# Kernel optimization log

Measured on AMD Instinct MI355X. Metric: run time of the kernel, lower is better.

The kernel has to match this reference:

```python
import jax, jax.numpy as jnp
import numpy as np

N = 100000      # n_nodes
E = 1600000     # n_edges (avg degree 16)
F_IN = 128      # nfeat
H = 128         # nhid
C = 64          # nclass


def setup_inputs() -> dict:
    key = jax.random.key(0)
    ks = jax.random.split(key, 6)
    x = jax.random.normal(ks[0], (N, F_IN), dtype=jnp.float32)
    edge_index = jax.random.randint(ks[1], (2, E), 0, N, dtype=jnp.int32)
    # Glorot-ish init for GCNConv weights, zeros for bias (PyG default)
    W1 = jax.random.normal(ks[2], (F_IN, H), dtype=jnp.float32) * (1.0 / np.sqrt(F_IN))
    b1 = jnp.zeros((H,), dtype=jnp.float32)
    W2 = jax.random.normal(ks[3], (H, C), dtype=jnp.float32) * (1.0 / np.sqrt(H))
    b2 = jnp.zeros((C,), dtype=jnp.float32)
    return {"x": x, "edge_index": edge_index, "W1": W1, "b1": b1, "W2": W2, "b2": b2}


def _gcn_conv(x, W, b, src, dst, n):
    """PyG GCNConv: h = W^T x, out_i = sum_j norm_ij * h_j + b, with
    symmetric normalization over the self-loop-augmented graph."""
    h = x @ W                                                   # [n, out]
    deg = jax.ops.segment_sum(jnp.ones(src.shape[0], h.dtype), dst, num_segments=n)
    dinv = jnp.where(deg > 0, jax.lax.rsqrt(deg), 0.0)          # D^-1/2
    norm = dinv[src] * dinv[dst]                                # [E+n]
    msg = h[src] * norm[:, None]                                # gather + scale
    out = jax.ops.segment_sum(msg, dst, num_segments=n)         # scatter-add
    return out + b


def reference(x, edge_index, W1, b1, W2, b2):
    loop = jnp.arange(N, dtype=edge_index.dtype)
    src = jnp.concatenate([edge_index[0], loop])  # sources j (with self loops)
    dst = jnp.concatenate([edge_index[1], loop])  # targets i
    h = jax.nn.relu(_gcn_conv(x, W1, b1, src, dst, N))  # dropout = identity (eval)
    out = _gcn_conv(h, W2, b2, src, dst, N)
    return jax.nn.log_softmax(out, axis=1)
```

## Files before the change

kernel.cpp:

```cpp
#include <hip/hip_runtime.h>
#include <hip/hip_fp16.h>
#include <cstdint>
#include <cstddef>
#include <cstring>


__device__ inline unsigned pack_bf16x2(float a, float b) {
    unsigned ua = __float_as_uint(a);
    unsigned ub = __float_as_uint(b);
    ua += 0x7fffu + ((ua >> 16) & 1u);
    ub += 0x7fffu + ((ub >> 16) & 1u);
    return (ua >> 16) | (ub & 0xffff0000u);
}
__device__ inline unsigned short bf16_rne(float v) {
    unsigned u = __float_as_uint(v);
    u += 0x7fffu + ((u >> 16) & 1u);
    return (unsigned short)(u >> 16);
}
__device__ inline float bf16lo(unsigned u) { return __uint_as_float(u << 16); }
__device__ inline float bf16hi(unsigned u) { return __uint_as_float(u & 0xffff0000u); }


typedef float fv2 __attribute__((ext_vector_type(2)));

template <bool HI>
__device__ inline fv2 fp8_fv2(unsigned u) {
#if __has_builtin(__builtin_amdgcn_cvt_pk_f32_fp8)
    return __builtin_amdgcn_cvt_pk_f32_fp8((int)u, HI);
#else
    unsigned u2 = HI ? (u >> 16) : (u & 0xffffu);
    unsigned w = (u2 & 0xFFu) | ((u2 & 0xFF00u) << 8);
    unsigned hb = ((w & 0x00800080u) << 8) | ((w & 0x007f007fu) << 7);
    __half2 h2;
    memcpy(&h2, &hb, 4);
    float2 f = __half22float2(h2);
    fv2 r;
    r.x = f.x * 256.0f;
    r.y = f.y * 256.0f;
    return r;
#endif
}

__device__ inline fv2 bfpair(unsigned u) {
    union { unsigned q[2]; fv2 f; } t;
    t.q[0] = u << 16;
    t.q[1] = u & 0xffff0000u;
    return t.f;
}

__device__ inline unsigned f32_to_fp8_byte(float v) {
    unsigned short hb = __half_as_ushort(__float2half(v * 0.00390625f));
    unsigned t = hb & 0x7fffu;
    t += 0x3fu + ((t >> 7) & 1u);
    return ((hb >> 8) & 0x80u) | (t >> 7);
}

__device__ inline unsigned char f32_to_fp8_b(float v) {
#if __has_builtin(__builtin_amdgcn_cvt_pk_fp8_f32)
    return (unsigned char)(__builtin_amdgcn_cvt_pk_fp8_f32(v, v, 0, false) & 0xff);
#else
    return (unsigned char)f32_to_fp8_byte(v);
#endif
}

typedef int iv4 __attribute__((ext_vector_type(4)));

#define NPART 8
#define KB    32
#define NPP_MAX 12500


__global__ void k_zero16(int* __restrict__ p) {
    if (threadIdx.x < 16) p[threadIdx.x] = 0;
}

__global__ __launch_bounds__(256) void k_bcount(const int* __restrict__ dst,
                                                int* __restrict__ bucketCount,
                                                int E, int npp) {
    __shared__ int c8[NPART];
    if (threadIdx.x < NPART) c8[threadIdx.x] = 0;
    __syncthreads();
    int t = blockIdx.x * blockDim.x + threadIdx.x;
    int stride = gridDim.x * blockDim.x;
    int E4 = E >> 2;
    const iv4* d4 = (const iv4*)dst;
    for (int i = t; i < E4; i += stride) {
        iv4 d = d4[i];
        atomicAdd(&c8[(unsigned)d.x / (unsigned)npp], 1);
        atomicAdd(&c8[(unsigned)d.y / (unsigned)npp], 1);
        atomicAdd(&c8[(unsigned)d.z / (unsigned)npp], 1);
        atomicAdd(&c8[(unsigned)d.w / (unsigned)npp], 1);
    }
    for (int e = E4 * 4 + t; e < E; e += stride)
        atomicAdd(&c8[(unsigned)dst[e] / (unsigned)npp], 1);
    __syncthreads();
    if (threadIdx.x < NPART) atomicAdd(&bucketCount[threadIdx.x], c8[threadIdx.x]);
}

__global__ void k_bscan(const int* __restrict__ bucketCount,
                        int* __restrict__ bucketBase,
                        int* __restrict__ bucketCursor) {
    if (threadIdx.x == 0) {
        int run = 0;
        for (int p = 0; p < NPART; ++p) {
            bucketBase[p] = run;
            bucketCursor[p] = run;
            run += bucketCount[p];
        }
    }
}

__global__ __launch_bounds__(256) void k_bucket(const int* __restrict__ src,
                                                const int* __restrict__ dst,
                                                int* __restrict__ bucketCursor,
                                                int2* __restrict__ pairs,
                                                int E, int npp) {
    __shared__ int cnt8[NPART], run8[NPART], gbase8[NPART];
    int tid = threadIdx.x;
    int base_e = blockIdx.x * 4096 + tid * 16;
    int nv = min(16, E - base_e);
    if (nv < 0) nv = 0;
    int dv[16], sv[16];
    if (nv == 16) {
        for (int q = 0; q < 4; ++q) {
            iv4 d = *(const iv4*)(dst + base_e + q * 4);
            iv4 s = *(const iv4*)(src + base_e + q * 4);
            dv[q * 4 + 0] = d.x; dv[q * 4 + 1] = d.y; dv[q * 4 + 2] = d.z; dv[q * 4 + 3] = d.w;
            sv[q * 4 + 0] = s.x; sv[q * 4 + 1] = s.y; sv[q * 4 + 2] = s.z; sv[q * 4 + 3] = s.w;
        }
    } else {
        for (int k = 0; k < nv; ++k) { dv[k] = dst[base_e + k]; sv[k] = src[base_e + k]; }
    }
    if (tid < NPART) { cnt8[tid] = 0; run8[tid] = 0; }
    __syncthreads();
    for (int k = 0; k < nv; ++k)
        atomicAdd(&cnt8[(unsigned)dv[k] / (unsigned)npp], 1);
    __syncthreads();
    if (tid < NPART) gbase8[tid] = atomicAdd(&bucketCursor[tid], cnt8[tid]);
    __syncthreads();
    for (int k = 0; k < nv; ++k) {
        int p = (unsigned)dv[k] / (unsigned)npp;
        int r = atomicAdd(&run8[p], 1);
        int2 pr; pr.x = dv[k]; pr.y = sv[k];
        pairs[gbase8[p] + r] = pr;
    }
}

__global__ __launch_bounds__(256) void k_count_part(const int2* __restrict__ pairs,
                                                    const int* __restrict__ bucketBase,
                                                    const int* __restrict__ bucketCount,
                                                    int* __restrict__ cntarr, int npp) {
    __shared__ int h[NPP_MAX];
    int p = blockIdx.x & (NPART - 1);
    int b = blockIdx.x >> 3;
    int lo = p * npp;
    for (int i = threadIdx.x; i < npp; i += 256) h[i] = 0;
    __syncthreads();
    int segBase = bucketBase[p], sz = bucketCount[p];
    int chunk = (sz + KB - 1) / KB;
    int s0 = segBase + b * chunk;
    int s1 = min(segBase + sz, s0 + chunk);
    for (int i = s0 + threadIdx.x; i < s1; i += 256)
        atomicAdd(&h[pairs[i].x - lo], 1);
    __syncthreads();
    size_t out = (size_t)(p * KB + b) * npp;
    for (int i = threadIdx.x; i < npp; i += 256) cntarr[out + i] = h[i];
}

__global__ void k_indeg(const int* __restrict__ cntarr, int* __restrict__ indeg,
                        int n, int npp) {
    int d = blockIdx.x * blockDim.x + threadIdx.x;
    if (d >= n) return;
    int p = (unsigned)d / (unsigned)npp;
    int dl = d - p * npp;
    size_t base = (size_t)p * KB * npp + dl;
    int s = 0;
    for (int b = 0; b < KB; ++b) s += cntarr[base + (size_t)b * npp];
    indeg[d] = s;
}

__global__ void k_scan_local(const int* __restrict__ in, int* __restrict__ out,
                             int* __restrict__ partials, int n) {
    __shared__ int s[256];
    int t = threadIdx.x;
    int base = blockIdx.x * 1024 + t * 4;
    int v0 = (base + 0) < n ? in[base + 0] : 0;
    int v1 = (base + 1) < n ? in[base + 1] : 0;
    int v2 = (base + 2) < n ? in[base + 2] : 0;
    int v3 = (base + 3) < n ? in[base + 3] : 0;
    int sum = v0 + v1 + v2 + v3;
    s[t] = sum;
    __syncthreads();
    for (int off = 1; off < 256; off <<= 1) {
        int x = (t >= off) ? s[t - off] : 0;
        __syncthreads();
        s[t] += x;
        __syncthreads();
    }
    int excl = s[t] - sum;
    if ((base + 0) < n) out[base + 0] = excl;
    if ((base + 1) < n) out[base + 1] = excl + v0;
    if ((base + 2) < n) out[base + 2] = excl + v0 + v1;
    if ((base + 3) < n) out[base + 3] = excl + v0 + v1 + v2;
    if (t == 255) partials[blockIdx.x] = s[255];
}

__global__ void k_scan_partials(int* __restrict__ partials, int np) {
    __shared__ int s[256];
    int t = threadIdx.x;
    int v = (t < np) ? partials[t] : 0;
    s[t] = v;
    __syncthreads();
    for (int off = 1; off < 256; off <<= 1) {
        int x = (t >= off) ? s[t - off] : 0;
        __syncthreads();
        s[t] += x;
        __syncthreads();
    }
    if (t < np) partials[t] = s[t] - v;
}

__global__ void k_finalize(int* __restrict__ row_ptr, const int* __restrict__ partials,
                           const int* __restrict__ indeg, float* __restrict__ dinv,
                           int n, int E) {
    int i = blockIdx.x * blockDim.x + threadIdx.x;
    if (i < n) {
        int rp = row_ptr[i] + partials[i >> 10];
        row_ptr[i] = rp;
        dinv[i] = rsqrtf((float)indeg[i] + 1.0f);
        if (i == 0) row_ptr[n] = E;
    }
}

__global__ void k_bases(int* __restrict__ cntarr, const int* __restrict__ row_ptr,
                        int n, int npp) {
    int d = blockIdx.x * blockDim.x + threadIdx.x;
    if (d >= n) return;
    int p = (unsigned)d / (unsigned)npp;
    int dl = d - p * npp;
    size_t base = (size_t)p * KB * npp + dl;
    int run = row_ptr[d];
    for (int b = 0; b < KB; ++b) {
        size_t idx = base + (size_t)b * npp;
        int c = cntarr[idx];
        cntarr[idx] = run;
        run += c;
    }
}

__global__ __launch_bounds__(256) void k_fill2(const int2* __restrict__ pairs,
                                               const int* __restrict__ bucketBase,
                                               const int* __restrict__ bucketCount,
                                               const int* __restrict__ cntarr,
                                               int* __restrict__ col, int npp) {
    __shared__ int cur[NPP_MAX];
    int p = blockIdx.x & (NPART - 1);
    int b = blockIdx.x >> 3;
    int lo = p * npp;
    size_t slice = (size_t)(p * KB + b) * npp;
    for (int i = threadIdx.x; i < npp; i += 256) cur[i] = cntarr[slice + i];
    __syncthreads();
    int segBase = bucketBase[p], sz = bucketCount[p];
    int chunk = (sz + KB - 1) / KB;
    int s0 = segBase + b * chunk;
    int s1 = min(segBase + sz, s0 + chunk);
    for (int i = s0 + threadIdx.x; i < s1; i += 256) {
        int2 e = pairs[i];
        int pos = atomicAdd(&cur[e.x - lo], 1);
        col[pos] = e.y;
    }
}

typedef __attribute__((ext_vector_type(8))) short short8;
typedef __attribute__((ext_vector_type(4))) float f32x4;

union FragU {
    short8 s;
    uint4 u4;
    unsigned u[4];
};

template <int NOUT>
__global__ void k_packW(const float* __restrict__ W, unsigned* __restrict__ Bp) {
    const int NT = NOUT / 16;
    int nf = 4 * NT * 64;
    for (int fid = threadIdx.x; fid < nf; fid += 256) {
        int q = fid / (NT * 64);
        int rem = fid - q * NT * 64;
        int nt = rem >> 6;
        int lane = rem & 63;
        int k0 = q * 32 + (lane >> 4) * 8;
        int ncol = nt * 16 + (lane & 15);
        unsigned u[4];
        for (int h = 0; h < 4; ++h) {
            float a = W[(k0 + 2 * h) * NOUT + ncol];
            float b = W[(k0 + 2 * h + 1) * NOUT + ncol];
            u[h] = pack_bf16x2(a, b);
        }
        uint4 o = {u[0], u[1], u[2], u[3]};
        *(uint4*)(Bp + (size_t)fid * 4) = o;
    }
}

__global__ __launch_bounds__(256) void k_gemm128_mfma(const float* __restrict__ X,
                                                      const unsigned* __restrict__ Bp,
                                                      const float* __restrict__ dinv,
                                                      unsigned char* __restrict__ H8,
                                                      int n) {
    int w = threadIdx.x >> 6;
    int lane = threadIdx.x & 63;
    int quad = lane >> 4;
    int lrow = lane & 15;
    int row0 = blockIdx.x * 64 + w * 16;
    int rowA = min(row0 + lrow, n - 1);

    f32x4 acc[8];
    for (int nt = 0; nt < 8; ++nt) acc[nt] = (f32x4){0.f, 0.f, 0.f, 0.f};

    for (int q = 0; q < 4; ++q) {
        const float* xp = X + (size_t)rowA * 128 + q * 32 + quad * 8;
        float4 x0 = *(const float4*)xp;
        float4 x1 = *(const float4*)(xp + 4);
        FragU a;
        a.u[0] = pack_bf16x2(x0.x, x0.y);
        a.u[1] = pack_bf16x2(x0.z, x0.w);
        a.u[2] = pack_bf16x2(x1.x, x1.y);
        a.u[3] = pack_bf16x2(x1.z, x1.w);
        for (int nt = 0; nt < 8; ++nt) {
            FragU b;
            b.u4 = *(const uint4*)(Bp + ((size_t)(q * 8 + nt) * 64 + lane) * 4);
            acc[nt] = __builtin_amdgcn_mfma_f32_16x16x32_bf16(a.s, b.s, acc[nt], 0, 0, 0);
        }
    }

    int rbase = row0 + quad * 4;
    float dv[4];
    if (rbase + 3 < n) {
        float4 d4 = *(const float4*)(dinv + rbase);
        dv[0] = d4.x; dv[1] = d4.y; dv[2] = d4.z; dv[3] = d4.w;
    } else {
        for (int r = 0; r < 4; ++r) dv[r] = dinv[min(rbase + r, n - 1)];
    }
    for (int nt = 0; nt < 8; ++nt) {
        for (int r = 0; r < 4; ++r) {
            int row = rbase + r;
            if (row < n)
                H8[(size_t)row * 128 + nt * 16 + lrow] = f32_to_fp8_b(dv[r] * acc[nt][r]);
        }
    }
}

__global__ __launch_bounds__(256) void k_gemm64_mfma(const unsigned* __restrict__ Xb,
                                                     const unsigned* __restrict__ Bp,
                                                     const float* __restrict__ dinv,
                                                     unsigned short* __restrict__ H16,
                                                     int n) {
    int w = threadIdx.x >> 6;
    int lane = threadIdx.x & 63;
    int quad = lane >> 4;
    int lrow = lane & 15;
    int row0 = blockIdx.x * 64 + w * 16;
    int rowA = min(row0 + lrow, n - 1);

    f32x4 acc[4];
    for (int nt = 0; nt < 4; ++nt) acc[nt] = (f32x4){0.f, 0.f, 0.f, 0.f};

    for (int q = 0; q < 4; ++q) {
        FragU a;
        a.u4 = *(const uint4*)(Xb + (size_t)rowA * 64 + q * 16 + quad * 4);
        for (int nt = 0; nt < 4; ++nt) {
            FragU b;
            b.u4 = *(const uint4*)(Bp + ((size_t)(q * 4 + nt) * 64 + lane) * 4);
            acc[nt] = __builtin_amdgcn_mfma_f32_16x16x32_bf16(a.s, b.s, acc[nt], 0, 0, 0);
        }
    }

    int rbase = row0 + quad * 4;
    float dv[4];
    if (rbase + 3 < n) {
        float4 d4 = *(const float4*)(dinv + rbase);
        dv[0] = d4.x; dv[1] = d4.y; dv[2] = d4.z; dv[3] = d4.w;
    } else {
        for (int r = 0; r < 4; ++r) dv[r] = dinv[min(rbase + r, n - 1)];
    }
    for (int nt = 0; nt < 4; ++nt) {
        for (int r = 0; r < 4; ++r) {
            int row = rbase + r;
            if (row < n)
                H16[(size_t)row * 64 + nt * 16 + lrow] = bf16_rne(dv[r] * acc[nt][r]);
        }
    }
}


__global__ __launch_bounds__(256) void k_agg_relu(const unsigned* __restrict__ hs,
                                                  const float* __restrict__ dinv,
                                                  const int* __restrict__ row_ptr,
                                                  const int* __restrict__ col,
                                                  const float* __restrict__ bias,
                                                  unsigned* __restrict__ out, int n) {
    int node = blockIdx.x * 16 + (threadIdx.x >> 4);
    if (node >= n) return;
    int l = threadIdx.x & 15;
    const uint2* hrow = (const uint2*)hs;
    fv2 a0 = {0.f, 0.f}, a1 = {0.f, 0.f}, a2 = {0.f, 0.f}, a3 = {0.f, 0.f};
    {
        uint2 u = hrow[(size_t)node * 16 + l];
        a0 += fp8_fv2<false>(u.x); a1 += fp8_fv2<true>(u.x);
        a2 += fp8_fv2<false>(u.y); a3 += fp8_fv2<true>(u.y);
    }
    int k = row_ptr[node], p1 = row_ptr[node + 1];
    for (; k + 8 <= p1; k += 8) {
        int cA = col[k + 0], cB = col[k + 1], cC = col[k + 2], cD = col[k + 3];
        int cE = col[k + 4], cF = col[k + 5], cG = col[k + 6], cH = col[k + 7];
        uint2 uA = hrow[(size_t)cA * 16 + l];
        uint2 uB = hrow[(size_t)cB * 16 + l];
        uint2 uC = hrow[(size_t)cC * 16 + l];
        uint2 uD = hrow[(size_t)cD * 16 + l];
        uint2 uE = hrow[(size_t)cE * 16 + l];
        uint2 uF = hrow[(size_t)cF * 16 + l];
        uint2 uG = hrow[(size_t)cG * 16 + l];
        uint2 uH = hrow[(size_t)cH * 16 + l];
        a0 += fp8_fv2<false>(uA.x); a1 += fp8_fv2<true>(uA.x);
        a2 += fp8_fv2<false>(uA.y); a3 += fp8_fv2<true>(uA.y);
        a0 += fp8_fv2<false>(uB.x); a1 += fp8_fv2<true>(uB.x);
        a2 += fp8_fv2<false>(uB.y); a3 += fp8_fv2<true>(uB.y);
        a0 += fp8_fv2<false>(uC.x); a1 += fp8_fv2<true>(uC.x);
        a2 += fp8_fv2<false>(uC.y); a3 += fp8_fv2<true>(uC.y);
        a0 += fp8_fv2<false>(uD.x); a1 += fp8_fv2<true>(uD.x);
        a2 += fp8_fv2<false>(uD.y); a3 += fp8_fv2<true>(uD.y);
        a0 += fp8_fv2<false>(uE.x); a1 += fp8_fv2<true>(uE.x);
        a2 += fp8_fv2<false>(uE.y); a3 += fp8_fv2<true>(uE.y);
        a0 += fp8_fv2<false>(uF.x); a1 += fp8_fv2<true>(uF.x);
        a2 += fp8_fv2<false>(uF.y); a3 += fp8_fv2<true>(uF.y);
        a0 += fp8_fv2<false>(uG.x); a1 += fp8_fv2<true>(uG.x);
        a2 += fp8_fv2<false>(uG.y); a3 += fp8_fv2<true>(uG.y);
        a0 += fp8_fv2<false>(uH.x); a1 += fp8_fv2<true>(uH.x);
        a2 += fp8_fv2<false>(uH.y); a3 += fp8_fv2<true>(uH.y);
    }
    for (; k + 4 <= p1; k += 4) {
        int cA = col[k + 0], cB = col[k + 1], cC = col[k + 2], cD = col[k + 3];
        uint2 uA = hrow[(size_t)cA * 16 + l];
        uint2 uB = hrow[(size_t)cB * 16 + l];
        uint2 uC = hrow[(size_t)cC * 16 + l];
        uint2 uD = hrow[(size_t)cD * 16 + l];
        a0 += fp8_fv2<false>(uA.x); a1 += fp8_fv2<true>(uA.x);
        a2 += fp8_fv2<false>(uA.y); a3 += fp8_fv2<true>(uA.y);
        a0 += fp8_fv2<false>(uB.x); a1 += fp8_fv2<true>(uB.x);
        a2 += fp8_fv2<false>(uB.y); a3 += fp8_fv2<true>(uB.y);
        a0 += fp8_fv2<false>(uC.x); a1 += fp8_fv2<true>(uC.x);
        a2 += fp8_fv2<false>(uC.y); a3 += fp8_fv2<true>(uC.y);
        a0 += fp8_fv2<false>(uD.x); a1 += fp8_fv2<true>(uD.x);
        a2 += fp8_fv2<false>(uD.y); a3 += fp8_fv2<true>(uD.y);
    }
    for (; k < p1; ++k) {
        int j = col[k];
        uint2 u = hrow[(size_t)j * 16 + l];
        a0 += fp8_fv2<false>(u.x); a1 += fp8_fv2<true>(u.x);
        a2 += fp8_fv2<false>(u.y); a3 += fp8_fv2<true>(u.y);
    }
    float di = dinv[node];
    float4 b4a = *(const float4*)(bias + 8 * l);
    float4 b4b = *(const float4*)(bias + 8 * l + 4);
    float v0 = fmaf(di, a0.x, b4a.x);
    float v1 = fmaf(di, a0.y, b4a.y);
    float v2 = fmaf(di, a1.x, b4a.z);
    float v3 = fmaf(di, a1.y, b4a.w);
    float v4 = fmaf(di, a2.x, b4b.x);
    float v5 = fmaf(di, a2.y, b4b.y);
    float v6 = fmaf(di, a3.x, b4b.z);
    float v7 = fmaf(di, a3.y, b4b.w);
    v0 = v0 > 0.f ? v0 : 0.f;
    v1 = v1 > 0.f ? v1 : 0.f;
    v2 = v2 > 0.f ? v2 : 0.f;
    v3 = v3 > 0.f ? v3 : 0.f;
    v4 = v4 > 0.f ? v4 : 0.f;
    v5 = v5 > 0.f ? v5 : 0.f;
    v6 = v6 > 0.f ? v6 : 0.f;
    v7 = v7 > 0.f ? v7 : 0.f;
    uint4 o = {pack_bf16x2(v0, v1), pack_bf16x2(v2, v3),
               pack_bf16x2(v4, v5), pack_bf16x2(v6, v7)};
    *(uint4*)(out + (size_t)node * 64 + 4 * l) = o;
}

__global__ __launch_bounds__(256) void k_agg_lsm(const unsigned* __restrict__ hs,
                                                 const float* __restrict__ dinv,
                                                 const int* __restrict__ row_ptr,
                                                 const int* __restrict__ col,
                                                 const float* __restrict__ bias,
                                                 float* __restrict__ out, int n) {
    int node = blockIdx.x * 16 + (threadIdx.x >> 4);
    if (node >= n) return;
    int l = threadIdx.x & 15;
    const uint2* hrow = (const uint2*)hs;
    fv2 aX = {0.f, 0.f}, aY = {0.f, 0.f};
    {
        uint2 u = hrow[(size_t)node * 16 + l];
        aX += bfpair(u.x);
        aY += bfpair(u.y);
    }
    int k = row_ptr[node], p1 = row_ptr[node + 1];
    for (; k + 8 <= p1; k += 8) {
        int cA = col[k + 0], cB = col[k + 1], cC = col[k + 2], cD = col[k + 3];
        int cE = col[k + 4], cF = col[k + 5], cG = col[k + 6], cH = col[k + 7];
        uint2 uA = hrow[(size_t)cA * 16 + l];
        uint2 uB = hrow[(size_t)cB * 16 + l];
        uint2 uC = hrow[(size_t)cC * 16 + l];
        uint2 uD = hrow[(size_t)cD * 16 + l];
        uint2 uE = hrow[(size_t)cE * 16 + l];
        uint2 uF = hrow[(size_t)cF * 16 + l];
        uint2 uG = hrow[(size_t)cG * 16 + l];
        uint2 uH = hrow[(size_t)cH * 16 + l];
        aX += bfpair(uA.x); aY += bfpair(uA.y);
        aX += bfpair(uB.x); aY += bfpair(uB.y);
        aX += bfpair(uC.x); aY += bfpair(uC.y);
        aX += bfpair(uD.x); aY += bfpair(uD.y);
        aX += bfpair(uE.x); aY += bfpair(uE.y);
        aX += bfpair(uF.x); aY += bfpair(uF.y);
        aX += bfpair(uG.x); aY += bfpair(uG.y);
        aX += bfpair(uH.x); aY += bfpair(uH.y);
    }
    for (; k + 4 <= p1; k += 4) {
        int cA = col[k + 0], cB = col[k + 1], cC = col[k + 2], cD = col[k + 3];
        uint2 uA = hrow[(size_t)cA * 16 + l];
        uint2 uB = hrow[(size_t)cB * 16 + l];
        uint2 uC = hrow[(size_t)cC * 16 + l];
        uint2 uD = hrow[(size_t)cD * 16 + l];
        aX += bfpair(uA.x); aY += bfpair(uA.y);
        aX += bfpair(uB.x); aY += bfpair(uB.y);
        aX += bfpair(uC.x); aY += bfpair(uC.y);
        aX += bfpair(uD.x); aY += bfpair(uD.y);
    }
    for (; k < p1; ++k) {
        int j = col[k];
        uint2 u = hrow[(size_t)j * 16 + l];
        aX += bfpair(u.x); aY += bfpair(u.y);
    }
    float di = dinv[node];
    float4 b4 = *(const float4*)(bias + 4 * l);
    float v0 = fmaf(di, aX.x, b4.x);
    float v1 = fmaf(di, aX.y, b4.y);
    float v2 = fmaf(di, aY.x, b4.z);
    float v3 = fmaf(di, aY.y, b4.w);
    float m = fmaxf(fmaxf(v0, v1), fmaxf(v2, v3));
    for (int off = 8; off; off >>= 1) m = fmaxf(m, __shfl_xor(m, off));
    float s = __expf(v0 - m) + __expf(v1 - m) + __expf(v2 - m) + __expf(v3 - m);
    for (int off = 8; off; off >>= 1) s += __shfl_xor(s, off);
    float ls = __logf(s);
    float4 o = {v0 - m - ls, v1 - m - ls, v2 - m - ls, v3 - m - ls};
    *(float4*)(out + (size_t)node * 64 + 4 * l) = o;
}


extern "C" void kernel_launch(void* const* d_in, const int* in_sizes, int n_in,
                              void* d_out, int out_size, void* d_ws, size_t ws_size,
                              hipStream_t stream) {
    const float* x  = (const float*)d_in[0];
    const int*   ei = (const int*)d_in[1];
    const float* W1 = (const float*)d_in[2];
    const float* b1 = (const float*)d_in[3];
    const float* W2 = (const float*)d_in[4];
    const float* b2 = (const float*)d_in[5];
    float* out = (float*)d_out;

    const int N = in_sizes[0] / 128;
    const int E = in_sizes[1] / 2;
    const int* src = ei;
    const int* dst = ei + E;
    const int npp = (N + NPART - 1) / NPART;

    char* w = (char*)d_ws;
    size_t off = 0;
    auto alloc = [&](size_t bytes) -> void* {
        void* p = w + off;
        off += (bytes + 255) & ~(size_t)255;
        return p;
    };
    int*      indeg    = (int*)alloc((size_t)N * 4);
    int*      row_ptr  = (int*)alloc((size_t)(N + 1) * 4);
    int*      colarr   = (int*)alloc((size_t)E * 4);
    int*      partials = (int*)alloc(256 * 4);
    int*      bmeta    = (int*)alloc(16 * 4);
    int*      bbase    = (int*)alloc(NPART * 4);
    float*    dinv     = (float*)alloc((size_t)N * 4);
    unsigned* h1f8     = (unsigned*)alloc((size_t)N * 32 * 4);
    unsigned* a1b      = (unsigned*)alloc((size_t)N * 64 * 4);
    unsigned* h2b      = (unsigned*)alloc((size_t)N * 32 * 4);
    unsigned* Bp1      = (unsigned*)alloc(4 * 8 * 64 * 16);
    unsigned* Bp2      = (unsigned*)alloc(4 * 4 * 64 * 16);
    int2* pairs  = (int2*)a1b;
    int*  cntarr = (int*)((char*)a1b + (size_t)E * 8);
    (void)ws_size; (void)n_in; (void)out_size;

    int* bucketCount  = bmeta;
    int* bucketCursor = bmeta + 8;
    int nscan = (N + 1023) / 1024;
    int nA3 = (E + 4095) / 4096;
    int ngemm = (N + 63) / 64;

    k_zero16<<<1, 64, 0, stream>>>(bmeta);
    k_packW<128><<<1, 256, 0, stream>>>(W1, Bp1);
    k_packW<64><<<1, 256, 0, stream>>>(W2, Bp2);
    k_bcount<<<256, 256, 0, stream>>>(dst, bucketCount, E, npp);
    k_bscan<<<1, 64, 0, stream>>>(bucketCount, bbase, bucketCursor);
    k_bucket<<<nA3, 256, 0, stream>>>(src, dst, bucketCursor, pairs, E, npp);
    k_count_part<<<NPART * KB, 256, 0, stream>>>(pairs, bbase, bucketCount, cntarr, npp);
    k_indeg<<<(N + 255) / 256, 256, 0, stream>>>(cntarr, indeg, N, npp);
    k_scan_local<<<nscan, 256, 0, stream>>>(indeg, row_ptr, partials, N);
    k_scan_partials<<<1, 256, 0, stream>>>(partials, nscan);
    k_finalize<<<(N + 255) / 256, 256, 0, stream>>>(row_ptr, partials, indeg, dinv, N, E);
    k_bases<<<(N + 255) / 256, 256, 0, stream>>>(cntarr, row_ptr, N, npp);
    k_fill2<<<NPART * KB, 256, 0, stream>>>(pairs, bbase, bucketCount, cntarr,
                                            colarr, npp);

    k_gemm128_mfma<<<ngemm, 256, 0, stream>>>(x, Bp1, dinv, (unsigned char*)h1f8, N);
    k_agg_relu<<<(N + 15) / 16, 256, 0, stream>>>(h1f8, dinv, row_ptr, colarr, b1, a1b, N);
    k_gemm64_mfma<<<ngemm, 256, 0, stream>>>(a1b, Bp2, dinv, (unsigned short*)h2b, N);
    k_agg_lsm<<<(N + 15) / 16, 256, 0, stream>>>(h2b, dinv, row_ptr, colarr, b2, out, N);
}
```

Baseline: 273.7 us.

## Replace partitioned bucket CSR build with direct global-atomic degree count and fill

```diff
diff --git a/kernel.cpp b/kernel.cpp
--- a/kernel.cpp
+++ b/kernel.cpp
@@ -65,118 +65,22 @@
 
 typedef int iv4 __attribute__((ext_vector_type(4)));
 
-#define NPART 8
-#define KB    32
-#define NPP_MAX 12500
-
-
-__global__ void k_zero16(int* __restrict__ p) {
-    if (threadIdx.x < 16) p[threadIdx.x] = 0;
-}
-
-__global__ __launch_bounds__(256) void k_bcount(const int* __restrict__ dst,
-                                                int* __restrict__ bucketCount,
-                                                int E, int npp) {
-    __shared__ int c8[NPART];
-    if (threadIdx.x < NPART) c8[threadIdx.x] = 0;
-    __syncthreads();
+
+__global__ __launch_bounds__(256) void k_deg(const int* __restrict__ dst,
+                                             int* __restrict__ indeg, int E) {
     int t = blockIdx.x * blockDim.x + threadIdx.x;
     int stride = gridDim.x * blockDim.x;
     int E4 = E >> 2;
     const iv4* d4 = (const iv4*)dst;
     for (int i = t; i < E4; i += stride) {
         iv4 d = d4[i];
-        atomicAdd(&c8[(unsigned)d.x / (unsigned)npp], 1);
-        atomicAdd(&c8[(unsigned)d.y / (unsigned)npp], 1);
-        atomicAdd(&c8[(unsigned)d.z / (unsigned)npp], 1);
-        atomicAdd(&c8[(unsigned)d.w / (unsigned)npp], 1);
+        atomicAdd(&indeg[d.x], 1);
+        atomicAdd(&indeg[d.y], 1);
+        atomicAdd(&indeg[d.z], 1);
+        atomicAdd(&indeg[d.w], 1);
     }
     for (int e = E4 * 4 + t; e < E; e += stride)
-        atomicAdd(&c8[(unsigned)dst[e] / (unsigned)npp], 1);
-    __syncthreads();
-    if (threadIdx.x < NPART) atomicAdd(&bucketCount[threadIdx.x], c8[threadIdx.x]);
-}
-
-__global__ void k_bscan(const int* __restrict__ bucketCount,
-                        int* __restrict__ bucketBase,
-                        int* __restrict__ bucketCursor) {
-    if (threadIdx.x == 0) {
-        int run = 0;
-        for (int p = 0; p < NPART; ++p) {
-            bucketBase[p] = run;
-            bucketCursor[p] = run;
-            run += bucketCount[p];
-        }
-    }
-}
-
-__global__ __launch_bounds__(256) void k_bucket(const int* __restrict__ src,
-                                                const int* __restrict__ dst,
-                                                int* __restrict__ bucketCursor,
-                                                int2* __restrict__ pairs,
-                                                int E, int npp) {
-    __shared__ int cnt8[NPART], run8[NPART], gbase8[NPART];
-    int tid = threadIdx.x;
-    int base_e = blockIdx.x * 4096 + tid * 16;
-    int nv = min(16, E - base_e);
-    if (nv < 0) nv = 0;
-    int dv[16], sv[16];
-    if (nv == 16) {
-        for (int q = 0; q < 4; ++q) {
-            iv4 d = *(const iv4*)(dst + base_e + q * 4);
-            iv4 s = *(const iv4*)(src + base_e + q * 4);
-            dv[q * 4 + 0] = d.x; dv[q * 4 + 1] = d.y; dv[q * 4 + 2] = d.z; dv[q * 4 + 3] = d.w;
-            sv[q * 4 + 0] = s.x; sv[q * 4 + 1] = s.y; sv[q * 4 + 2] = s.z; sv[q * 4 + 3] = s.w;
-        }
-    } else {
-        for (int k = 0; k < nv; ++k) { dv[k] = dst[base_e + k]; sv[k] = src[base_e + k]; }
-    }
-    if (tid < NPART) { cnt8[tid] = 0; run8[tid] = 0; }
-    __syncthreads();
-    for (int k = 0; k < nv; ++k)
-        atomicAdd(&cnt8[(unsigned)dv[k] / (unsigned)npp], 1);
-    __syncthreads();
-    if (tid < NPART) gbase8[tid] = atomicAdd(&bucketCursor[tid], cnt8[tid]);
-    __syncthreads();
-    for (int k = 0; k < nv; ++k) {
-        int p = (unsigned)dv[k] / (unsigned)npp;
-        int r = atomicAdd(&run8[p], 1);
-        int2 pr; pr.x = dv[k]; pr.y = sv[k];
-        pairs[gbase8[p] + r] = pr;
-    }
-}
-
-__global__ __launch_bounds__(256) void k_count_part(const int2* __restrict__ pairs,
-                                                    const int* __restrict__ bucketBase,
-                                                    const int* __restrict__ bucketCount,
-                                                    int* __restrict__ cntarr, int npp) {
-    __shared__ int h[NPP_MAX];
-    int p = blockIdx.x & (NPART - 1);
-    int b = blockIdx.x >> 3;
-    int lo = p * npp;
-    for (int i = threadIdx.x; i < npp; i += 256) h[i] = 0;
-    __syncthreads();
-    int segBase = bucketBase[p], sz = bucketCount[p];
-    int chunk = (sz + KB - 1) / KB;
-    int s0 = segBase + b * chunk;
-    int s1 = min(segBase + sz, s0 + chunk);
-    for (int i = s0 + threadIdx.x; i < s1; i += 256)
-        atomicAdd(&h[pairs[i].x - lo], 1);
-    __syncthreads();
-    size_t out = (size_t)(p * KB + b) * npp;
-    for (int i = threadIdx.x; i < npp; i += 256) cntarr[out + i] = h[i];
-}
-
-__global__ void k_indeg(const int* __restrict__ cntarr, int* __restrict__ indeg,
-                        int n, int npp) {
-    int d = blockIdx.x * blockDim.x + threadIdx.x;
-    if (d >= n) return;
-    int p = (unsigned)d / (unsigned)npp;
-    int dl = d - p * npp;
-    size_t base = (size_t)p * KB * npp + dl;
-    int s = 0;
-    for (int b = 0; b < KB; ++b) s += cntarr[base + (size_t)b * npp];
-    indeg[d] = s;
+        atomicAdd(&indeg[dst[e]], 1);
 }
 
 __global__ void k_scan_local(const int* __restrict__ in, int* __restrict__ out,
@@ -221,54 +125,37 @@
 }
 
 __global__ void k_finalize(int* __restrict__ row_ptr, const int* __restrict__ partials,
-                           const int* __restrict__ indeg, float* __restrict__ dinv,
+                           int* __restrict__ indeg, float* __restrict__ dinv,
                            int n, int E) {
     int i = blockIdx.x * blockDim.x + threadIdx.x;
     if (i < n) {
         int rp = row_ptr[i] + partials[i >> 10];
         row_ptr[i] = rp;
         dinv[i] = rsqrtf((float)indeg[i] + 1.0f);
+        indeg[i] = rp;
         if (i == 0) row_ptr[n] = E;
     }
 }
 
-__global__ void k_bases(int* __restrict__ cntarr, const int* __restrict__ row_ptr,
-                        int n, int npp) {
-    int d = blockIdx.x * blockDim.x + threadIdx.x;
-    if (d >= n) return;
-    int p = (unsigned)d / (unsigned)npp;
-    int dl = d - p * npp;
-    size_t base = (size_t)p * KB * npp + dl;
-    int run = row_ptr[d];
-    for (int b = 0; b < KB; ++b) {
-        size_t idx = base + (size_t)b * npp;
-        int c = cntarr[idx];
-        cntarr[idx] = run;
-        run += c;
-    }
-}
-
-__global__ __launch_bounds__(256) void k_fill2(const int2* __restrict__ pairs,
-                                               const int* __restrict__ bucketBase,
-                                               const int* __restrict__ bucketCount,
-                                               const int* __restrict__ cntarr,
-                                               int* __restrict__ col, int npp) {
-    __shared__ int cur[NPP_MAX];
-    int p = blockIdx.x & (NPART - 1);
-    int b = blockIdx.x >> 3;
-    int lo = p * npp;
-    size_t slice = (size_t)(p * KB + b) * npp;
-    for (int i = threadIdx.x; i < npp; i += 256) cur[i] = cntarr[slice + i];
-    __syncthreads();
-    int segBase = bucketBase[p], sz = bucketCount[p];
-    int chunk = (sz + KB - 1) / KB;
-    int s0 = segBase + b * chunk;
-    int s1 = min(segBase + sz, s0 + chunk);
-    for (int i = s0 + threadIdx.x; i < s1; i += 256) {
-        int2 e = pairs[i];
-        int pos = atomicAdd(&cur[e.x - lo], 1);
-        col[pos] = e.y;
-    }
+__global__ __launch_bounds__(256) void k_fill(const int* __restrict__ src,
+                                              const int* __restrict__ dst,
+                                              int* __restrict__ cursor,
+                                              int* __restrict__ col, int E) {
+    int t = blockIdx.x * blockDim.x + threadIdx.x;
+    int stride = gridDim.x * blockDim.x;
+    int E4 = E >> 2;
+    const iv4* d4 = (const iv4*)dst;
+    const iv4* s4 = (const iv4*)src;
+    for (int i = t; i < E4; i += stride) {
+        iv4 d = d4[i];
+        iv4 s = s4[i];
+        col[atomicAdd(&cursor[d.x], 1)] = s.x;
+        col[atomicAdd(&cursor[d.y], 1)] = s.y;
+        col[atomicAdd(&cursor[d.z], 1)] = s.z;
+        col[atomicAdd(&cursor[d.w], 1)] = s.w;
+    }
+    for (int e = E4 * 4 + t; e < E; e += stride)
+        col[atomicAdd(&cursor[dst[e]], 1)] = src[e];
 }
 
 typedef __attribute__((ext_vector_type(8))) short short8;
@@ -567,7 +454,6 @@
     const int E = in_sizes[1] / 2;
     const int* src = ei;
     const int* dst = ei + E;
-    const int npp = (N + NPART - 1) / NPART;
 
     char* w = (char*)d_ws;
     size_t off = 0;
@@ -580,38 +466,25 @@
     int*      row_ptr  = (int*)alloc((size_t)(N + 1) * 4);
     int*      colarr   = (int*)alloc((size_t)E * 4);
     int*      partials = (int*)alloc(256 * 4);
-    int*      bmeta    = (int*)alloc(16 * 4);
-    int*      bbase    = (int*)alloc(NPART * 4);
     float*    dinv     = (float*)alloc((size_t)N * 4);
     unsigned* h1f8     = (unsigned*)alloc((size_t)N * 32 * 4);
     unsigned* a1b      = (unsigned*)alloc((size_t)N * 64 * 4);
     unsigned* h2b      = (unsigned*)alloc((size_t)N * 32 * 4);
     unsigned* Bp1      = (unsigned*)alloc(4 * 8 * 64 * 16);
     unsigned* Bp2      = (unsigned*)alloc(4 * 4 * 64 * 16);
-    int2* pairs  = (int2*)a1b;
-    int*  cntarr = (int*)((char*)a1b + (size_t)E * 8);
     (void)ws_size; (void)n_in; (void)out_size;
 
-    int* bucketCount  = bmeta;
-    int* bucketCursor = bmeta + 8;
     int nscan = (N + 1023) / 1024;
-    int nA3 = (E + 4095) / 4096;
     int ngemm = (N + 63) / 64;
 
-    k_zero16<<<1, 64, 0, stream>>>(bmeta);
+    hipMemsetAsync(indeg, 0, (size_t)N * 4, stream);
     k_packW<128><<<1, 256, 0, stream>>>(W1, Bp1);
     k_packW<64><<<1, 256, 0, stream>>>(W2, Bp2);
-    k_bcount<<<256, 256, 0, stream>>>(dst, bucketCount, E, npp);
-    k_bscan<<<1, 64, 0, stream>>>(bucketCount, bbase, bucketCursor);
-    k_bucket<<<nA3, 256, 0, stream>>>(src, dst, bucketCursor, pairs, E, npp);
-    k_count_part<<<NPART * KB, 256, 0, stream>>>(pairs, bbase, bucketCount, cntarr, npp);
-    k_indeg<<<(N + 255) / 256, 256, 0, stream>>>(cntarr, indeg, N, npp);
+    k_deg<<<512, 256, 0, stream>>>(dst, indeg, E);
     k_scan_local<<<nscan, 256, 0, stream>>>(indeg, row_ptr, partials, N);
     k_scan_partials<<<1, 256, 0, stream>>>(partials, nscan);
     k_finalize<<<(N + 255) / 256, 256, 0, stream>>>(row_ptr, partials, indeg, dinv, N, E);
-    k_bases<<<(N + 255) / 256, 256, 0, stream>>>(cntarr, row_ptr, N, npp);
-    k_fill2<<<NPART * KB, 256, 0, stream>>>(pairs, bbase, bucketCount, cntarr,
-                                            colarr, npp);
+    k_fill<<<512, 256, 0, stream>>>(src, dst, indeg, colarr, E);
 
     k_gemm128_mfma<<<ngemm, 256, 0, stream>>>(x, Bp1, dinv, (unsigned char*)h1f8, N);
     k_agg_relu<<<(N + 15) / 16, 256, 0, stream>>>(h1f8, dinv, row_ptr, colarr, b1, a1b, N);
```

After: 391.8 us. 1.43x slower.
